# Kernel tuning notes

Hardware: AMD Instinct MI355X
Metric: run time of the kernel (lower is better)

## Reference

```python
import jax, jax.numpy as jnp
import numpy as np

E = 512
H = 8
HD = E // H
EPS = 1e-5


def setup_inputs() -> dict:
    key = jax.random.key(0)
    ks = jax.random.split(key, 12)
    S, B = 2048, 4
    bound_in = float(np.sqrt(6.0 / (3 * E + E)))  # xavier_uniform for in_proj
    inp = {
        "x": jax.random.normal(ks[0], (S, B, E), dtype=jnp.float32),
        "in_proj_weight": jax.random.uniform(ks[1], (3 * E, E), minval=-bound_in, maxval=bound_in, dtype=jnp.float32),
        "in_proj_bias": jnp.zeros((3 * E,), jnp.float32),
        "out_proj_weight": jax.random.normal(ks[2], (E, E), dtype=jnp.float32) * 0.02,
        "out_proj_bias": jnp.zeros((E,), jnp.float32),
        "ln1_gamma": jnp.ones((E,), jnp.float32),
        "ln1_beta": jnp.zeros((E,), jnp.float32),
        "fc1_weight": jax.random.normal(ks[3], (4 * E, E), dtype=jnp.float32) * 0.02,
        "fc1_bias": jnp.zeros((4 * E,), jnp.float32),
        "fc2_weight": jax.random.normal(ks[4], (E, 4 * E), dtype=jnp.float32) * 0.02,
        "fc2_bias": jnp.zeros((E,), jnp.float32),
        "ln2_gamma": jnp.ones((E,), jnp.float32),
        "ln2_beta": jnp.zeros((E,), jnp.float32),
    }
    return inp


def _layer_norm(x, gamma, beta):
    mu = jnp.mean(x, axis=-1, keepdims=True)
    var = jnp.mean(jnp.square(x - mu), axis=-1, keepdims=True)
    return (x - mu) * jax.lax.rsqrt(var + EPS) * gamma + beta


def _encoder_layer(x, in_w, in_b, out_w, out_b, g1, b1, fc1_w, fc1_b, fc2_w, fc2_b, g2, b2):
    S, B, _ = x.shape
    # --- self attention (hand-rolled, full S x S scores as in original) ---
    qkv = x @ in_w.T + in_b                      # [S, B, 3E]
    q, k, v = jnp.split(qkv, 3, axis=-1)         # each [S, B, E]
    # [S, B, E] -> [B*H, S, HD]
    def to_heads(t):
        return t.reshape(S, B * H, HD).transpose(1, 0, 2)
    q, k, v = to_heads(q), to_heads(k), to_heads(v)
    scores = jnp.einsum('bsd,btd->bst', q, k) / jnp.sqrt(jnp.float32(HD))  # [B*H, S, S]
    attn_w = jax.nn.softmax(scores, axis=-1)
    attn = jnp.einsum('bst,btd->bsd', attn_w, v)  # [B*H, S, HD]
    attn = attn.transpose(1, 0, 2).reshape(S, B, E)
    attn = attn @ out_w.T + out_b
    # --- residual + LN ---
    x = _layer_norm(x + attn, g1, b1)
    # --- FFN ---
    h = jax.nn.relu(x @ fc1_w.T + fc1_b)
    h = h @ fc2_w.T + fc2_b
    return _layer_norm(x + h, g2, b2)


def reference(x, in_proj_weight, in_proj_bias, out_proj_weight, out_proj_bias,
              ln1_gamma, ln1_beta, fc1_weight, fc1_bias, fc2_weight, fc2_bias,
              ln2_gamma, ln2_beta):
    return _encoder_layer(x, in_proj_weight, in_proj_bias, out_proj_weight, out_proj_bias,
                          ln1_gamma, ln1_beta, fc1_weight, fc1_bias, fc2_weight, fc2_bias,
                          ln2_gamma, ln2_beta)
```

## Files before the change

### kernel.cpp

```cpp
#include <hip/hip_runtime.h>

typedef _Float16 half8 __attribute__((ext_vector_type(8)));
typedef _Float16 half4 __attribute__((ext_vector_type(4)));
typedef float f32x4 __attribute__((ext_vector_type(4)));

static __device__ __forceinline__ f32x4 mfma16(half8 a, half8 b, f32x4 c) {
    return __builtin_amdgcn_mfma_f32_16x16x32_f16(a, b, c, 0, 0, 0);
}

static __device__ __forceinline__ void gload16(const void* g, const void* l) {
    __builtin_amdgcn_global_load_lds(
        (const __attribute__((address_space(1))) unsigned int*)(unsigned long long)g,
        (__attribute__((address_space(3))) unsigned int*)(unsigned int)(unsigned long long)l,
        16, 0, 0);
}

template <int N> static __device__ __forceinline__ void waitcnt_vm() {
    if constexpr (N == 0)      asm volatile("s_waitcnt vmcnt(0)" ::: "memory");
    else if constexpr (N == 2) asm volatile("s_waitcnt vmcnt(2)" ::: "memory");
    else if constexpr (N == 3) asm volatile("s_waitcnt vmcnt(3)" ::: "memory");
    else if constexpr (N == 4) asm volatile("s_waitcnt vmcnt(4)" ::: "memory");
    else if constexpr (N == 6) asm volatile("s_waitcnt vmcnt(6)" ::: "memory");
    else if constexpr (N == 8) asm volatile("s_waitcnt vmcnt(8)" ::: "memory");
}

__global__ void __launch_bounds__(256) conv_all(const float* __restrict__ x,
                                                const float* __restrict__ inw,
                                                const float* __restrict__ outw,
                                                const float* __restrict__ f1w,
                                                const float* __restrict__ f2w,
                                                _Float16* __restrict__ X16,
                                                _Float16* __restrict__ WIN,
                                                _Float16* __restrict__ WOUT,
                                                _Float16* __restrict__ WF1,
                                                _Float16* __restrict__ WF2) {
    const int bid = blockIdx.x;
    const float* src;
    _Float16* dst;
    long base;
    if (bid < 2048)      { src = x;    dst = X16;  base = (long)bid * 2048; }
    else if (bid < 2432) { src = inw;  dst = WIN;  base = (long)(bid - 2048) * 2048; }
    else if (bid < 2560) { src = outw; dst = WOUT; base = (long)(bid - 2432) * 2048; }
    else if (bid < 3072) { src = f1w;  dst = WF1;  base = (long)(bid - 2560) * 2048; }
    else                 { src = f2w;  dst = WF2;  base = (long)(bid - 3072) * 2048; }
    const long i = base + threadIdx.x * 8;
    f32x4 v0 = *(const f32x4*)(src + i);
    f32x4 v1 = *(const f32x4*)(src + i + 4);
    half8 h;
#pragma unroll
    for (int j = 0; j < 4; j++) { h[j] = (_Float16)v0[j]; h[4 + j] = (_Float16)v1[j]; }
    *(half8*)(dst + i) = h;
}

template <int MODE, int MI, int NI>
__global__ void __launch_bounds__(256) gemm_bt(const _Float16* __restrict__ A,
                                               const _Float16* __restrict__ Bw,
                                               const float* __restrict__ bias,
                                               const float* __restrict__ resid,
                                               void* __restrict__ Cout,
                                               int M, int N, int K) {
    constexpr int L = MI / 2 + NI / 2;
    __shared__ __align__(16) _Float16 As[3][32 * MI * 32];
    __shared__ __align__(16) _Float16 Bs[3][32 * NI * 32];
    const int tid = threadIdx.x;
    const int lane = tid & 63;
    const int w = tid >> 6;
    const int g = lane >> 4, l15 = lane & 15;
    const int wm = w >> 1, wn = w & 1;
    const long rowblk = (long)blockIdx.y * (32 * MI);
    const long colblk = (long)blockIdx.x * (32 * NI);

    const int lrow = lane >> 2;
    const int lcol = (lane & 3) * 8;

    f32x4 zero = {0.f, 0.f, 0.f, 0.f};
    f32x4 acc[MI][NI];
#pragma unroll
    for (int i = 0; i < MI; i++)
#pragma unroll
        for (int j = 0; j < NI; j++) acc[i][j] = zero;

    auto stage = [&](int k0, int bufi) {
#pragma unroll
        for (int a = 0; a < MI / 2; a++)
            gload16(A + (rowblk + w * (8 * MI) + a * 16 + lrow) * (long)K + k0 + lcol,
                    As[bufi] + (w * (8 * MI) + a * 16) * 32);
#pragma unroll
        for (int c = 0; c < NI / 2; c++)
            gload16(Bw + (colblk + w * (8 * NI) + c * 16 + lrow) * (long)K + k0 + lcol,
                    Bs[bufi] + (w * (8 * NI) + c * 16) * 32);
    };

    stage(0, 0);
    if (32 < K) stage(32, 1);
    int cur = 0;
    for (int k0 = 0; k0 < K; k0 += 32) {
        if (k0 + 64 < K) {
            int nxt = cur + 2; if (nxt >= 3) nxt -= 3;
            stage(k0 + 64, nxt);
            waitcnt_vm<2 * L>();
        } else if (k0 + 32 < K) {
            waitcnt_vm<L>();
        } else {
            waitcnt_vm<0>();
        }
        __builtin_amdgcn_s_barrier();
        half8 af[MI], bf[NI];
#pragma unroll
        for (int mi = 0; mi < MI; mi++)
            af[mi] = *(const half8*)(As[cur] + (wm * (16 * MI) + mi * 16 + l15) * 32 + g * 8);
#pragma unroll
        for (int ni = 0; ni < NI; ni++)
            bf[ni] = *(const half8*)(Bs[cur] + (wn * (16 * NI) + ni * 16 + l15) * 32 + g * 8);
#pragma unroll
        for (int mi = 0; mi < MI; mi++)
#pragma unroll
            for (int ni = 0; ni < NI; ni++)
                acc[mi][ni] = mfma16(bf[ni], af[mi], acc[mi][ni]);
        __builtin_amdgcn_s_barrier();
        cur = (cur == 2) ? 0 : cur + 1;
    }

#pragma unroll
    for (int mi = 0; mi < MI; mi++) {
        const long m = rowblk + wm * (16 * MI) + mi * 16 + l15;
#pragma unroll
        for (int ni = 0; ni < NI; ni++) {
            const long n0 = colblk + wn * (16 * NI) + ni * 16 + g * 4;
            const f32x4 bb = *(const f32x4*)(bias + n0);
            f32x4 v = acc[mi][ni] + bb;
            if (MODE == 1) {
#pragma unroll
                for (int r = 0; r < 4; r++) v[r] = fmaxf(v[r], 0.f);
            }
            if (MODE == 2) {
                const f32x4 rv = *(const f32x4*)(resid + m * N + n0);
                *(f32x4*)((float*)Cout + m * N + n0) = v + rv;
            } else if (MODE == 3) {
                const long sel = n0 >> 9;
                const int hh = (int)(n0 >> 6) & 7;
                const int d0 = (int)n0 & 63;
                const int ss = (int)(m >> 2), b = (int)m & 3;
                if (sel == 0) v *= 0.18033688f;
                half4 hv;
#pragma unroll
                for (int r = 0; r < 4; r++) hv[r] = (_Float16)v[r];
                *(half4*)((_Float16*)Cout + sel * (32L * 2048 * 64) +
                          ((long)(b * 8 + hh) * 2048 + ss) * 64 + d0) = hv;
            } else {
                half4 hv;
#pragma unroll
                for (int r = 0; r < 4; r++) hv[r] = (_Float16)v[r];
                *(half4*)((_Float16*)Cout + m * N + n0) = hv;
            }
        }
    }
    (void)M;
}

__global__ void __launch_bounds__(256) transpose_v(const _Float16* __restrict__ Vh,
                                                   _Float16* __restrict__ Vt) {
    __shared__ _Float16 T[64][72];
    const int tid = threadIdx.x;
    const int bh = blockIdx.y;
    const int t0 = blockIdx.x * 64;
    const _Float16* src = Vh + ((long)bh * 2048 + t0) * 64;
    const int row = tid >> 2, col = (tid & 3) * 16;
    *(half8*)&T[row][col] = *(const half8*)(src + row * 64 + col);
    *(half8*)&T[row][col + 8] = *(const half8*)(src + row * 64 + col + 8);
    __syncthreads();
    const int d = tid >> 2, tc = (tid & 3) * 16;
    half8 a, b;
#pragma unroll
    for (int j = 0; j < 8; j++) { a[j] = T[tc + j][d]; b[j] = T[tc + 8 + j][d]; }
    _Float16* dst = Vt + ((long)bh * 64 + d) * 2048 + t0 + tc;
    *(half8*)dst = a;
    *(half8*)(dst + 8) = b;
}

__global__ void __launch_bounds__(256) attn_fwd(const _Float16* __restrict__ Qh,
                                                const _Float16* __restrict__ Kh,
                                                const _Float16* __restrict__ Vt,
                                                _Float16* __restrict__ out) {
    __shared__ __align__(16) _Float16 Klds[2][64 * 64];
    __shared__ __align__(16) _Float16 Vlds[2][64 * 64];
    __shared__ __align__(16) _Float16 Plds[4][16 * 64];
    const int tid = threadIdx.x;
    const int lane = tid & 63;
    const int w = tid >> 6;
    const int g = lane >> 4, l15 = lane & 15;
    const int bh = blockIdx.y;
    const int b = bh >> 3, h = bh & 7;
    const int s0 = blockIdx.x * 64 + w * 16;
    const _Float16* Qb = Qh + (long)bh * 2048 * 64;
    const _Float16* Kb = Kh + (long)bh * 2048 * 64;
    const _Float16* Vb = Vt + (long)bh * 64 * 2048;

    const int srow = lane >> 3;
    const int scolb = (lane & 7) * 16;

    half8 qb[2];
#pragma unroll
    for (int ks = 0; ks < 2; ks++)
        qb[ks] = *(const half8*)(Qb + (s0 + l15) * 64 + ks * 32 + g * 8);

    f32x4 zero = {0.f, 0.f, 0.f, 0.f};
    f32x4 ot[4];
#pragma unroll
    for (int di = 0; di < 4; di++) ot[di] = zero;
    float lsum = 0.f;

    auto stage = [&](int t0, int buf) {
#pragma unroll
        for (int j = 0; j < 2; j++) {
            const int row = w * 16 + j * 8 + srow;
            const int src = scolb ^ ((row & 7) << 4);
            gload16(Kb + (long)(t0 + row) * 64 + (src >> 1),
                    Klds[buf] + (w * 16 + j * 8) * 64);
            gload16(Vb + (long)row * 2048 + t0 + (src >> 1),
                    Vlds[buf] + (w * 16 + j * 8) * 64);
        }
    };

    stage(0, 0);
    __syncthreads();
    int buf = 0;

    for (int t0 = 0; t0 < 2048; t0 += 64) {
        if (t0 + 64 < 2048) stage(t0 + 64, buf ^ 1);

        __builtin_amdgcn_s_setprio(1);
        f32x4 st[4];
#pragma unroll
        for (int ni = 0; ni < 4; ni++) {
            st[ni] = zero;
#pragma unroll
            for (int ks = 0; ks < 2; ks++) {
                const int t = ni * 16 + l15;
                const int cb = (ks * 64 + g * 16) ^ ((t & 7) << 4);
                half8 ka = *(const half8*)((const char*)Klds[buf] + t * 128 + cb);
                st[ni] = mfma16(ka, qb[ks], st[ni]);
            }
        }
        __builtin_amdgcn_s_setprio(0);

        char* const pw = (char*)Plds[w] + l15 * 128;
#pragma unroll
        for (int ni = 0; ni < 4; ni++) {
            half4 pv4;
#pragma unroll
            for (int r = 0; r < 4; r++) {
                const float pe = __builtin_exp2f(st[ni][r]);
                lsum += pe;
                pv4[r] = (_Float16)pe;
            }
            *(half4*)(pw + ((ni * 32 + g * 8) ^ ((l15 & 7) << 4))) = pv4;
        }

        half8 pa[2];
#pragma unroll
        for (int ks = 0; ks < 2; ks++)
            pa[ks] = *(const half8*)(pw + ((ks * 64 + g * 16) ^ ((l15 & 7) << 4)));
        __builtin_amdgcn_s_setprio(1);
#pragma unroll
        for (int di = 0; di < 4; di++)
#pragma unroll
            for (int ks = 0; ks < 2; ks++) {
                const int d = di * 16 + l15;
                const int cb = (ks * 64 + g * 16) ^ ((d & 7) << 4);
                half8 vb = *(const half8*)((const char*)Vlds[buf] + d * 128 + cb);
                ot[di] = mfma16(vb, pa[ks], ot[di]);
            }
        __builtin_amdgcn_s_setprio(0);

        __syncthreads();
        buf ^= 1;
    }

    lsum += __shfl_xor(lsum, 16);
    lsum += __shfl_xor(lsum, 32);
    const float inv = 1.f / lsum;
    const long q = s0 + l15;
#pragma unroll
    for (int di = 0; di < 4; di++) {
        half4 hv;
#pragma unroll
        for (int r = 0; r < 4; r++) hv[r] = (_Float16)(ot[di][r] * inv);
        *(half4*)(out + (q * 4 + b) * 512 + h * 64 + di * 16 + g * 4) = hv;
    }
}

__global__ void __launch_bounds__(256) ln_rows(const float* __restrict__ in,
                                               const float* __restrict__ gamma,
                                               const float* __restrict__ beta,
                                               float* __restrict__ outf,
                                               _Float16* __restrict__ outh) {
    const int tid = threadIdx.x, lane = tid & 63, w = tid >> 6;
    const long row = (long)blockIdx.x * 4 + w;
    const float* p = in + row * 512 + lane * 8;
    f32x4 v0 = *(const f32x4*)p;
    f32x4 v1 = *(const f32x4*)(p + 4);
    float s = v0[0] + v0[1] + v0[2] + v0[3] + v1[0] + v1[1] + v1[2] + v1[3];
    float q = v0[0] * v0[0] + v0[1] * v0[1] + v0[2] * v0[2] + v0[3] * v0[3] +
              v1[0] * v1[0] + v1[1] * v1[1] + v1[2] * v1[2] + v1[3] * v1[3];
#pragma unroll
    for (int off = 1; off < 64; off <<= 1) {
        s += __shfl_xor(s, off);
        q += __shfl_xor(q, off);
    }
    const float mu = s * (1.0f / 512.0f);
    const float var = q * (1.0f / 512.0f) - mu * mu;
    const float rstd = rsqrtf(var + 1e-5f);
    const float* gp = gamma + lane * 8;
    const float* bp = beta + lane * 8;
    f32x4 g0 = *(const f32x4*)gp, g1 = *(const f32x4*)(gp + 4);
    f32x4 b0 = *(const f32x4*)bp, b1 = *(const f32x4*)(bp + 4);
    f32x4 o0, o1;
#pragma unroll
    for (int j = 0; j < 4; j++) {
        o0[j] = (v0[j] - mu) * rstd * g0[j] + b0[j];
        o1[j] = (v1[j] - mu) * rstd * g1[j] + b1[j];
    }
    float* op = outf + row * 512 + lane * 8;
    *(f32x4*)op = o0;
    *(f32x4*)(op + 4) = o1;
    if (outh) {
        half8 hh;
#pragma unroll
        for (int j = 0; j < 4; j++) { hh[j] = (_Float16)o0[j]; hh[4 + j] = (_Float16)o1[j]; }
        *(half8*)(outh + row * 512 + lane * 8) = hh;
    }
}

extern "C" void kernel_launch(void* const* d_in, const int* in_sizes, int n_in,
                              void* d_out, int out_size, void* d_ws, size_t ws_size,
                              hipStream_t stream) {
    const float* x    = (const float*)d_in[0];
    const float* inw  = (const float*)d_in[1];
    const float* inb  = (const float*)d_in[2];
    const float* outw = (const float*)d_in[3];
    const float* outb = (const float*)d_in[4];
    const float* g1   = (const float*)d_in[5];
    const float* b1   = (const float*)d_in[6];
    const float* f1w  = (const float*)d_in[7];
    const float* f1b  = (const float*)d_in[8];
    const float* f2w  = (const float*)d_in[9];
    const float* f2b  = (const float*)d_in[10];
    const float* g2   = (const float*)d_in[11];
    const float* b2   = (const float*)d_in[12];

    char* ws = (char*)d_ws;
    const long MB = 1024 * 1024;
    _Float16* X16   = (_Float16*)(ws + 0);
    _Float16* HEADS = (_Float16*)(ws + 8 * MB);
    _Float16* H16   = (_Float16*)(ws + 0);
    _Float16* VT    = (_Float16*)(ws + 32 * MB);
    _Float16* ATT   = (_Float16*)(ws + 40 * MB);
    float*    PRE   = (float*)(ws + 48 * MB);
    float*    YF    = (float*)(ws + 64 * MB);
    _Float16* Y16   = (_Float16*)(ws + 80 * MB);
    _Float16* WIN   = (_Float16*)(ws + 88 * MB);
    _Float16* WOUT  = (_Float16*)(ws + 90 * MB);
    _Float16* WF1   = (_Float16*)(ws + 91 * MB);
    _Float16* WF2   = (_Float16*)(ws + 93 * MB);

    _Float16* Qh = HEADS;
    _Float16* Kh = HEADS + 32L * 2048 * 64;
    _Float16* Vh = HEADS + 2 * 32L * 2048 * 64;

    conv_all<<<3584, 256, 0, stream>>>(x, inw, outw, f1w, f2w, X16, WIN, WOUT, WF1, WF2);

    gemm_bt<3, 4, 4><<<dim3(12, 64), 256, 0, stream>>>(X16, WIN, inb, nullptr, HEADS, 8192, 1536, 512);
    transpose_v<<<dim3(32, 32), 256, 0, stream>>>(Vh, VT);
    attn_fwd<<<dim3(32, 32), 256, 0, stream>>>(Qh, Kh, VT, ATT);
    gemm_bt<2, 2, 2><<<dim3(8, 128), 256, 0, stream>>>(ATT, WOUT, outb, x, PRE, 8192, 512, 512);
    ln_rows<<<2048, 256, 0, stream>>>(PRE, g1, b1, YF, Y16);
    gemm_bt<1, 4, 4><<<dim3(16, 64), 256, 0, stream>>>(Y16, WF1, f1b, nullptr, H16, 8192, 2048, 512);
    gemm_bt<2, 2, 2><<<dim3(8, 128), 256, 0, stream>>>(H16, WF2, f2b, YF, PRE, 8192, 512, 2048);
    ln_rows<<<2048, 256, 0, stream>>>(PRE, g2, b2, (float*)d_out, nullptr);
}
```

Measured before the change: 315.6 us.

## Switch GEMM to double-buffered pipeline, pack fp16 with cvt_pkrtz, retile N=512 GEMMs

The GEMM's three-stage LDS ring with partial vmcnt waits becomes a two-buffer scheme: the next tile is issued before the MFMAs, then a full vmcnt(0) wait and a barrier close each iteration. All float-to-half conversions (GEMM epilogues, attention P tile and output, LayerNorm fp16 output) now use packed round-toward-zero conversion instead of scalar casts. The out-projection and FC2 GEMMs use 4x2 tiles with half as many row blocks. The shallower pipeline exposes more load latency, and round-toward-zero changes rounding slightly.

```diff
diff --git a/kernel.cpp b/kernel.cpp
--- a/kernel.cpp
+++ b/kernel.cpp
@@ -6,6 +6,15 @@
 
 static __device__ __forceinline__ f32x4 mfma16(half8 a, half8 b, f32x4 c) {
     return __builtin_amdgcn_mfma_f32_16x16x32_f16(a, b, c, 0, 0, 0);
+}
+
+static __device__ __forceinline__ half4 pack4(f32x4 v) {
+    auto a = __builtin_amdgcn_cvt_pkrtz(v[0], v[1]);
+    auto b = __builtin_amdgcn_cvt_pkrtz(v[2], v[3]);
+    half4 r;
+    r[0] = (_Float16)a[0]; r[1] = (_Float16)a[1];
+    r[2] = (_Float16)b[0]; r[3] = (_Float16)b[1];
+    return r;
 }
 
 static __device__ __forceinline__ void gload16(const void* g, const void* l) {
@@ -13,15 +22,6 @@
         (const __attribute__((address_space(1))) unsigned int*)(unsigned long long)g,
         (__attribute__((address_space(3))) unsigned int*)(unsigned int)(unsigned long long)l,
         16, 0, 0);
-}
-
-template <int N> static __device__ __forceinline__ void waitcnt_vm() {
-    if constexpr (N == 0)      asm volatile("s_waitcnt vmcnt(0)" ::: "memory");
-    else if constexpr (N == 2) asm volatile("s_waitcnt vmcnt(2)" ::: "memory");
-    else if constexpr (N == 3) asm volatile("s_waitcnt vmcnt(3)" ::: "memory");
-    else if constexpr (N == 4) asm volatile("s_waitcnt vmcnt(4)" ::: "memory");
-    else if constexpr (N == 6) asm volatile("s_waitcnt vmcnt(6)" ::: "memory");
-    else if constexpr (N == 8) asm volatile("s_waitcnt vmcnt(8)" ::: "memory");
 }
 
 __global__ void __launch_bounds__(256) conv_all(const float* __restrict__ x,
@@ -59,9 +59,8 @@
                                                const float* __restrict__ resid,
                                                void* __restrict__ Cout,
                                                int M, int N, int K) {
-    constexpr int L = MI / 2 + NI / 2;
-    __shared__ __align__(16) _Float16 As[3][32 * MI * 32];
-    __shared__ __align__(16) _Float16 Bs[3][32 * NI * 32];
+    __shared__ __align__(16) _Float16 As[2][32 * MI * 32];
+    __shared__ __align__(16) _Float16 Bs[2][32 * NI * 32];
     const int tid = threadIdx.x;
     const int lane = tid & 63;
     const int w = tid >> 6;
@@ -92,19 +91,11 @@
     };
 
     stage(0, 0);
-    if (32 < K) stage(32, 1);
+    asm volatile("s_waitcnt vmcnt(0)" ::: "memory");
+    __builtin_amdgcn_s_barrier();
     int cur = 0;
     for (int k0 = 0; k0 < K; k0 += 32) {
-        if (k0 + 64 < K) {
-            int nxt = cur + 2; if (nxt >= 3) nxt -= 3;
-            stage(k0 + 64, nxt);
-            waitcnt_vm<2 * L>();
-        } else if (k0 + 32 < K) {
-            waitcnt_vm<L>();
-        } else {
-            waitcnt_vm<0>();
-        }
-        __builtin_amdgcn_s_barrier();
+        if (k0 + 32 < K) stage(k0 + 32, cur ^ 1);
         half8 af[MI], bf[NI];
 #pragma unroll
         for (int mi = 0; mi < MI; mi++)
@@ -117,8 +108,9 @@
 #pragma unroll
             for (int ni = 0; ni < NI; ni++)
                 acc[mi][ni] = mfma16(bf[ni], af[mi], acc[mi][ni]);
+        asm volatile("s_waitcnt vmcnt(0)" ::: "memory");
         __builtin_amdgcn_s_barrier();
-        cur = (cur == 2) ? 0 : cur + 1;
+        cur ^= 1;
     }
 
 #pragma unroll
@@ -142,16 +134,10 @@
                 const int d0 = (int)n0 & 63;
                 const int ss = (int)(m >> 2), b = (int)m & 3;
                 if (sel == 0) v *= 0.18033688f;
-                half4 hv;
-#pragma unroll
-                for (int r = 0; r < 4; r++) hv[r] = (_Float16)v[r];
                 *(half4*)((_Float16*)Cout + sel * (32L * 2048 * 64) +
-                          ((long)(b * 8 + hh) * 2048 + ss) * 64 + d0) = hv;
+                          ((long)(b * 8 + hh) * 2048 + ss) * 64 + d0) = pack4(v);
             } else {
-                half4 hv;
-#pragma unroll
-                for (int r = 0; r < 4; r++) hv[r] = (_Float16)v[r];
-                *(half4*)((_Float16*)Cout + m * N + n0) = hv;
+                *(half4*)((_Float16*)Cout + m * N + n0) = pack4(v);
             }
         }
     }
@@ -247,14 +233,13 @@
         char* const pw = (char*)Plds[w] + l15 * 128;
 #pragma unroll
         for (int ni = 0; ni < 4; ni++) {
-            half4 pv4;
+            f32x4 pe;
 #pragma unroll
             for (int r = 0; r < 4; r++) {
-                const float pe = __builtin_exp2f(st[ni][r]);
-                lsum += pe;
-                pv4[r] = (_Float16)pe;
-            }
-            *(half4*)(pw + ((ni * 32 + g * 8) ^ ((l15 & 7) << 4))) = pv4;
+                pe[r] = __builtin_exp2f(st[ni][r]);
+                lsum += pe[r];
+            }
+            *(half4*)(pw + ((ni * 32 + g * 8) ^ ((l15 & 7) << 4))) = pack4(pe);
         }
 
         half8 pa[2];
@@ -283,10 +268,10 @@
     const long q = s0 + l15;
 #pragma unroll
     for (int di = 0; di < 4; di++) {
-        half4 hv;
-#pragma unroll
-        for (int r = 0; r < 4; r++) hv[r] = (_Float16)(ot[di][r] * inv);
-        *(half4*)(out + (q * 4 + b) * 512 + h * 64 + di * 16 + g * 4) = hv;
+        f32x4 v;
+#pragma unroll
+        for (int r = 0; r < 4; r++) v[r] = ot[di][r] * inv;
+        *(half4*)(out + (q * 4 + b) * 512 + h * 64 + di * 16 + g * 4) = pack4(v);
     }
 }
 
@@ -325,9 +310,10 @@
     *(f32x4*)op = o0;
     *(f32x4*)(op + 4) = o1;
     if (outh) {
+        half4 lo = pack4(o0), hi = pack4(o1);
         half8 hh;
 #pragma unroll
-        for (int j = 0; j < 4; j++) { hh[j] = (_Float16)o0[j]; hh[4 + j] = (_Float16)o1[j]; }
+        for (int j = 0; j < 4; j++) { hh[j] = lo[j]; hh[4 + j] = hi[j]; }
         *(half8*)(outh + row * 512 + lane * 8) = hh;
     }
 }
@@ -373,9 +359,9 @@
     gemm_bt<3, 4, 4><<<dim3(12, 64), 256, 0, stream>>>(X16, WIN, inb, nullptr, HEADS, 8192, 1536, 512);
     transpose_v<<<dim3(32, 32), 256, 0, stream>>>(Vh, VT);
     attn_fwd<<<dim3(32, 32), 256, 0, stream>>>(Qh, Kh, VT, ATT);
-    gemm_bt<2, 2, 2><<<dim3(8, 128), 256, 0, stream>>>(ATT, WOUT, outb, x, PRE, 8192, 512, 512);
+    gemm_bt<2, 4, 2><<<dim3(8, 64), 256, 0, stream>>>(ATT, WOUT, outb, x, PRE, 8192, 512, 512);
     ln_rows<<<2048, 256, 0, stream>>>(PRE, g1, b1, YF, Y16);
     gemm_bt<1, 4, 4><<<dim3(16, 64), 256, 0, stream>>>(Y16, WF1, f1b, nullptr, H16, 8192, 2048, 512);
-    gemm_bt<2, 2, 2><<<dim3(8, 128), 256, 0, stream>>>(H16, WF2, f2b, YF, PRE, 8192, 512, 2048);
+    gemm_bt<2, 4, 2><<<dim3(8, 64), 256, 0, stream>>>(H16, WF2, f2b, YF, PRE, 8192, 512, 2048);
     ln_rows<<<2048, 256, 0, stream>>>(PRE, g2, b2, (float*)d_out, nullptr);
 }
```

Result: faster. 307.8 us (-2.5%).
